# Kernel tuning notes

Hardware: AMD Instinct MI355X
Metric: run time of the kernel (lower is better)

The kernel has to match this reference:

```python
import jax, jax.numpy as jnp
import numpy as np

D = 256; NH = 8; NL = 4; NP = 4; NLAYERS = 6; DFF = 1024; DH = D // NH
B = 2
SHAPES = [(128, 128), (64, 64), (32, 32), (16, 16)]
S_TOTAL = sum(h * w for h, w in SHAPES)  # 21760


def setup_inputs() -> dict:
    key = jax.random.key(0)
    ks = iter(jax.random.split(key, 64))
    inp = {}
    for l, (h, w) in enumerate(SHAPES):
        inp[f"src{l}"] = jax.random.normal(next(ks), (B, D, h, w), jnp.float32)
        inp[f"pos{l}"] = jax.random.normal(next(ks), (B, D, h, w), jnp.float32)
    def p(shape):
        return jax.random.normal(next(ks), shape, jnp.float32) * 0.02
    inp["level_embed"] = p((NL, D))
    inp["Woff"] = p((NLAYERS, D, NH * NL * NP * 2)); inp["boff"] = p((NLAYERS, NH * NL * NP * 2))
    inp["Wattn"] = p((NLAYERS, D, NH * NL * NP)); inp["battn"] = p((NLAYERS, NH * NL * NP))
    inp["Wval"] = p((NLAYERS, D, D)); inp["bval"] = p((NLAYERS, D))
    inp["Wout"] = p((NLAYERS, D, D)); inp["bout"] = p((NLAYERS, D))
    inp["ln1_s"] = jnp.ones((NLAYERS, D)); inp["ln1_b"] = jnp.zeros((NLAYERS, D))
    inp["W1"] = p((NLAYERS, D, DFF)); inp["b1"] = p((NLAYERS, DFF))
    inp["W2"] = p((NLAYERS, DFF, D)); inp["b2"] = p((NLAYERS, D))
    inp["ln2_s"] = jnp.ones((NLAYERS, D)); inp["ln2_b"] = jnp.zeros((NLAYERS, D))
    return inp


def _layer_norm(x, s, b, eps=1e-5):
    m = jnp.mean(x, -1, keepdims=True)
    v = jnp.mean((x - m) ** 2, -1, keepdims=True)
    return (x - m) * jax.lax.rsqrt(v + eps) * s + b


def _ref_points(batch):
    # masks are all-False -> valid_ratios == 1, so reference points are just
    # normalized pixel centers, identical across the level axis.
    refs = []
    for h, w in SHAPES:
        yy, xx = jnp.meshgrid((jnp.arange(h) + 0.5) / h, (jnp.arange(w) + 0.5) / w, indexing="ij")
        refs.append(jnp.stack([xx.ravel(), yy.ravel()], -1))
    ref = jnp.concatenate(refs, 0)  # [S, 2] (x, y)
    return jnp.broadcast_to(ref[None, :, None, :], (batch, S_TOTAL, NL, 2))


def _ms_deform_attn(query, ref, src, Woff, boff, Wattn, battn, Wval, bval, Wout, bout):
    Bq, S, _ = query.shape
    value = (src @ Wval + bval).reshape(Bq, S, NH, DH)
    off = (query @ Woff + boff).reshape(Bq, S, NH, NL, NP, 2)
    aw = jax.nn.softmax((query @ Wattn + battn).reshape(Bq, S, NH, NL * NP), -1)
    aw = aw.reshape(Bq, S, NH, NL, NP)
    norm = jnp.array([[w, h] for h, w in SHAPES], dtype=query.dtype)  # [NL,2] = (W,H)
    loc = ref[:, :, None, :, None, :] + off / norm[None, None, None, :, None, :]  # [B,S,NH,NL,NP,2]
    out = jnp.zeros((Bq, NH, S, DH), query.dtype)
    start = 0
    for l, (h, w) in enumerate(SHAPES):
        v = value[:, start:start + h * w].transpose(0, 2, 1, 3)  # [B,NH,h*w,DH]
        start += h * w
        # grid_sample align_corners=False convention
        x = loc[:, :, :, l, :, 0] * w - 0.5  # [B,S,NH,NP]
        y = loc[:, :, :, l, :, 1] * h - 0.5
        x0 = jnp.floor(x); y0 = jnp.floor(y)
        lx = x - x0; ly = y - y0
        x0i = x0.astype(jnp.int32); y0i = y0.astype(jnp.int32)
        def tr(a):  # [B,S,NH,NP] -> [B,NH,S*NP,1]
            return a.transpose(0, 2, 1, 3).reshape(Bq, NH, S * NP, 1)
        def gather(xi, yi):
            ok = (xi >= 0) & (xi < w) & (yi >= 0) & (yi < h)
            idx = jnp.clip(yi, 0, h - 1) * w + jnp.clip(xi, 0, w - 1)
            idx = idx.transpose(0, 2, 1, 3).reshape(Bq, NH, S * NP)
            g = jnp.take_along_axis(v, idx[..., None], axis=2)  # [B,NH,S*NP,DH]
            return g * tr(ok).astype(v.dtype)  # zero padding outside
        samp = (tr((1 - lx) * (1 - ly)) * gather(x0i, y0i)
                + tr(lx * (1 - ly)) * gather(x0i + 1, y0i)
                + tr((1 - lx) * ly) * gather(x0i, y0i + 1)
                + tr(lx * ly) * gather(x0i + 1, y0i + 1))
        samp = (samp * tr(aw[:, :, :, l])).reshape(Bq, NH, S, NP, DH).sum(3)
        out = out + samp
    out = out.transpose(0, 2, 1, 3).reshape(Bq, S, D)
    return out @ Wout + bout


def _forward(srcs, poss, level_embed, Woff, boff, Wattn, battn, Wval, bval, Wout, bout,
             ln1_s, ln1_b, W1, b1, W2, b2, ln2_s, ln2_b):
    bsz = srcs[0].shape[0]
    src_flat = jnp.concatenate([s.reshape(bsz, D, -1).transpose(0, 2, 1) for s in srcs], 1)
    pos_flat = jnp.concatenate(
        [p.reshape(bsz, D, -1).transpose(0, 2, 1) + level_embed[l] for l, p in enumerate(poss)], 1)
    ref = _ref_points(bsz)
    out = src_flat
    for i in range(NLAYERS):
        q = out + pos_flat
        attn = _ms_deform_attn(q, ref, out, Woff[i], boff[i], Wattn[i], battn[i],
                               Wval[i], bval[i], Wout[i], bout[i])
        out = _layer_norm(out + attn, ln1_s[i], ln1_b[i])
        ff = jax.nn.relu(out @ W1[i] + b1[i]) @ W2[i] + b2[i]
        out = _layer_norm(out + ff, ln2_s[i], ln2_b[i])
    return out  # memory: [B, S_TOTAL, D]


def reference(src0, src1, src2, src3, pos0, pos1, pos2, pos3, level_embed,
              Woff, boff, Wattn, battn, Wval, bval, Wout, bout,
              ln1_s, ln1_b, W1, b1, W2, b2, ln2_s, ln2_b):
    return _forward([src0, src1, src2, src3], [pos0, pos1, pos2, pos3], level_embed,
                    Woff, boff, Wattn, battn, Wval, bval, Wout, bout,
                    ln1_s, ln1_b, W1, b1, W2, b2, ln2_s, ln2_b)
```

## Files before the change

kernel.cpp:

```cpp
#include <hip/hip_runtime.h>
#include <math.h>

#define DMODEL 256
#define NHEADS 8
#define NLAY 6
#define DFF 1024
#define DHEAD 32
#define NB 2
#define STOT 21760
#define MTOT (NB * STOT)

typedef unsigned short u16;
typedef __attribute__((ext_vector_type(8))) short short8;
typedef __attribute__((ext_vector_type(4))) float floatx4;

__device__ __forceinline__ float bf2f(u16 h) {
    unsigned int u = ((unsigned int)h) << 16;
    return __uint_as_float(u);
}
__device__ __forceinline__ u16 f2bf(float f) {
    unsigned int u = __float_as_uint(f);
    u = u + 0x7fffu + ((u >> 16) & 1u);
    return (u16)(u >> 16);
}

__global__ __launch_bounds__(256)
void biascat_kernel(const float* __restrict__ boff, const float* __restrict__ battn,
                    float* __restrict__ bias384)
{
    const int t = blockIdx.x * 256 + threadIdx.x;
    if (t >= NLAY * 384) return;
    const int i = t / 384, c = t - i * 384;
    bias384[t] = (c < 256) ? boff[i * 256 + c] : battn[i * 128 + (c - 256)];
}

__global__ __launch_bounds__(256)
void wtrans_kernel(const float* __restrict__ W, u16* __restrict__ Wt,
                   const int K, const int N, const long wstride, const long ostride)
{
    __shared__ float ts[32][33];
    W  += blockIdx.z * wstride;
    Wt += blockIdx.z * ostride;
    const int n0 = blockIdx.x * 32;
    const int k0 = blockIdx.y * 32;
    const int t = threadIdx.x;
    const int nl = t & 31, kl = t >> 5;
#pragma unroll
    for (int p = 0; p < 4; ++p) {
        const int k = kl + p * 8;
        ts[k][nl] = W[(long)(k0 + k) * N + n0 + nl];
    }
    __syncthreads();
    const int c = t & 31, r0 = t >> 5;
#pragma unroll
    for (int p = 0; p < 4; ++p) {
        const int r = r0 + p * 8;
        Wt[(long)(n0 + r) * K + k0 + c] = f2bf(ts[c][r]);
    }
}

__global__ __launch_bounds__(256)
void flatten_kernel(const float* __restrict__ src, const float* __restrict__ pos,
                    const float* __restrict__ le_row,
                    float* __restrict__ out, u16* __restrict__ outb,
                    u16* __restrict__ posb, u16* __restrict__ qb,
                    int HW, int start)
{
    __shared__ float ts[32][33];
    __shared__ float tp[32][33];
    const int b   = blockIdx.z;
    const int d0  = blockIdx.y * 32;
    const int hw0 = blockIdx.x * 32;
    const int t   = threadIdx.x;
    const int hwl = t & 31;
    const int dl  = t >> 5;
#pragma unroll
    for (int p = 0; p < 4; ++p) {
        const int dd = dl + p * 8;
        const int d  = d0 + dd;
        const long idx = ((long)(b * DMODEL + d)) * HW + hw0 + hwl;
        ts[dd][hwl] = src[idx];
        tp[dd][hwl] = pos[idx] + le_row[d];
    }
    __syncthreads();
    const int dl2  = t & 31;
    const int hwl2 = t >> 5;
#pragma unroll
    for (int p = 0; p < 4; ++p) {
        const int hh  = hwl2 + p * 8;
        const int tok = start + hw0 + hh;
        const long o  = ((long)(b * STOT + tok)) * DMODEL + d0 + dl2;
        const float v = ts[dl2][hh];
        const float pp = tp[dl2][hh];
        out[o]  = v;
        outb[o] = f2bf(v);
        posb[o] = f2bf(pp);
        qb[o]   = f2bf(v + pp);
    }
}

__global__ __launch_bounds__(256)
void mfma_gemm(const u16* __restrict__ A, const u16* __restrict__ Bt,
               const int ldb, const float* __restrict__ bias,
               u16* __restrict__ Cb, const int ldc, u16* __restrict__ Cb2,
               const int K, const int relu)
{
    __shared__ u16 As[128 * 40];
    __shared__ u16 Bs[128 * 40];
    const int tid  = threadIdx.x;
    const int wv   = tid >> 6;
    const int lane = tid & 63;
    const int m0 = blockIdx.y * 128;
    const int n0 = blockIdx.x * 128;
    const int wm = (wv & 1) * 64;
    const int wn = (wv >> 1) * 64;
    const int q   = lane >> 4;
    const int c16 = lane & 15;

    const int srow = tid >> 2;
    const int scol = (tid & 3) * 8;

    floatx4 acc[4][4];
#pragma unroll
    for (int i = 0; i < 4; ++i)
#pragma unroll
        for (int j = 0; j < 4; ++j)
            acc[i][j] = (floatx4){0.f, 0.f, 0.f, 0.f};

    union Frag { short8 v; uint2 u[2]; };

    for (int k0 = 0; k0 < K; k0 += 32) {
#pragma unroll
        for (int it = 0; it < 2; ++it) {
            const int r = srow + it * 64;
            const uint4 va = *(const uint4*)(A + (long)(m0 + r) * K + k0 + scol);
            uint2 lo, hi;
            lo.x = va.x; lo.y = va.y; hi.x = va.z; hi.y = va.w;
            *(uint2*)&As[r * 40 + scol]     = lo;
            *(uint2*)&As[r * 40 + scol + 4] = hi;
            const uint4 vb = *(const uint4*)(Bt + (long)(n0 + r) * ldb + k0 + scol);
            lo.x = vb.x; lo.y = vb.y; hi.x = vb.z; hi.y = vb.w;
            *(uint2*)&Bs[r * 40 + scol]     = lo;
            *(uint2*)&Bs[r * 40 + scol + 4] = hi;
        }
        __syncthreads();

        short8 af[4], bf[4];
#pragma unroll
        for (int i = 0; i < 4; ++i) {
            Frag fa;
            const int ao = (wm + i * 16 + c16) * 40 + q * 8;
            fa.u[0] = *(const uint2*)&As[ao];
            fa.u[1] = *(const uint2*)&As[ao + 4];
            af[i] = fa.v;
            Frag fb;
            const int bo = (wn + i * 16 + c16) * 40 + q * 8;
            fb.u[0] = *(const uint2*)&Bs[bo];
            fb.u[1] = *(const uint2*)&Bs[bo + 4];
            bf[i] = fb.v;
        }
#pragma unroll
        for (int i = 0; i < 4; ++i)
#pragma unroll
            for (int j = 0; j < 4; ++j)
                acc[i][j] = __builtin_amdgcn_mfma_f32_16x16x32_bf16(
                    af[i], bf[j], acc[i][j], 0, 0, 0);
        __syncthreads();
    }

    u16* cb  = Cb;
    int ldcb = ldc, csub = 0;
    if (Cb2 && n0 >= 256) { cb = Cb2; ldcb = 128; csub = 256; }

#pragma unroll
    for (int i = 0; i < 4; ++i) {
#pragma unroll
        for (int j = 0; j < 4; ++j) {
            const int col = n0 + wn + j * 16 + c16;
            const float bv = bias ? bias[col] : 0.f;
#pragma unroll
            for (int r = 0; r < 4; ++r) {
                const int row = m0 + wm + i * 16 + q * 4 + r;
                float v = acc[i][j][r] + bv;
                if (relu) v = fmaxf(v, 0.f);
                cb[(long)row * ldcb + col - csub] = f2bf(v);
            }
        }
    }
}

__global__ __launch_bounds__(256)
void sample_kernel(const u16* __restrict__ value, const u16* __restrict__ offb,
                   const u16* __restrict__ logit, u16* __restrict__ sb)
{
    constexpr int LW[4] = {128, 64, 32, 16};
    constexpr int SH[4] = {7, 6, 5, 4};
    constexpr int LS[4] = {0, 16384, 20480, 21504};

    const int t = threadIdx.x;
    const int tl = t >> 6;
    const int tid64 = t & 63;
    const int h = tid64 >> 3;
    const int lane8 = tid64 & 7;
    const int blk = blockIdx.x * 4 + tl;
    const int b = blk / STOT;
    const int s = blk - b * STOT;

    float refx, refy;
    if (s < 16384) {
        const int yy = s >> 7, xx = s & 127;
        refx = (xx + 0.5f) * (1.f / 128.f); refy = (yy + 0.5f) * (1.f / 128.f);
    } else if (s < 20480) {
        const int sl = s - 16384; const int yy = sl >> 6, xx = sl & 63;
        refx = (xx + 0.5f) * (1.f / 64.f);  refy = (yy + 0.5f) * (1.f / 64.f);
    } else if (s < 21504) {
        const int sl = s - 20480; const int yy = sl >> 5, xx = sl & 31;
        refx = (xx + 0.5f) * (1.f / 32.f);  refy = (yy + 0.5f) * (1.f / 32.f);
    } else {
        const int sl = s - 21504; const int yy = sl >> 4, xx = sl & 15;
        refx = (xx + 0.5f) * (1.f / 16.f);  refy = (yy + 0.5f) * (1.f / 16.f);
    }

    const uint* awp = (const uint*)(logit + (long)blk * 128 + h * 16);
    const uint4 la = ((const uint4*)awp)[0];
    const uint4 lb = ((const uint4*)awp)[1];
    const uint lu[8] = {la.x, la.y, la.z, la.w, lb.x, lb.y, lb.z, lb.w};
    float lv[16];
#pragma unroll
    for (int j = 0; j < 8; ++j) {
        lv[2 * j]     = bf2f((u16)(lu[j] & 0xffffu));
        lv[2 * j + 1] = bf2f((u16)(lu[j] >> 16));
    }
    float mx = lv[0];
#pragma unroll
    for (int i = 1; i < 16; ++i) mx = fmaxf(mx, lv[i]);
    float pw[16];
    float se = 0.f;
#pragma unroll
    for (int i = 0; i < 16; ++i) { pw[i] = __expf(lv[i] - mx); se += pw[i]; }
    const float inv = 1.f / se;

    const uint* offp = (const uint*)(offb + (long)blk * 256 + h * 32);
    const int ch = h * DHEAD + lane8 * 4;
    const u16* vtok = value + (long)b * STOT * DMODEL + ch;

    float a0 = 0.f, a1 = 0.f, a2 = 0.f, a3 = 0.f;
#pragma unroll
    for (int l = 0; l < 4; ++l) {
        const int lw = LW[l], sh = SH[l];
        const u16* vbase = vtok + (long)LS[l] * DMODEL;
        const uint4 olv = ((const uint4*)offp)[l];
        const uint ou[4] = {olv.x, olv.y, olv.z, olv.w};
        const float fx = refx * lw - 0.5f;
        const float fy = refy * lw - 0.5f;

        float w[16];
        int ofs[16];
#pragma unroll
        for (int p = 0; p < 4; ++p) {
            const uint o2 = ou[p];
            const float x = fx + bf2f((u16)(o2 & 0xffffu));
            const float y = fy + bf2f((u16)(o2 >> 16));
            const float x0f = floorf(x), y0f = floorf(y);
            const float lx = x - x0f, ly = y - y0f;
            const int x0 = (int)x0f, y0 = (int)y0f;
            const float aP = pw[l * 4 + p];
            const float wx0 = ((uint)x0 < (uint)lw) ? (1.f - lx) : 0.f;
            const float wx1 = ((uint)(x0 + 1) < (uint)lw) ? lx : 0.f;
            const float wy0 = ((uint)y0 < (uint)lw) ? (aP * (1.f - ly)) : 0.f;
            const float wy1 = ((uint)(y0 + 1) < (uint)lw) ? (aP * ly) : 0.f;
            const int xc0 = x0 & (lw - 1), xc1 = (x0 + 1) & (lw - 1);
            const int r0 = (y0 & (lw - 1)) << sh;
            const int r1 = ((y0 + 1) & (lw - 1)) << sh;
            w[p * 4 + 0] = wy0 * wx0; ofs[p * 4 + 0] = r0 + xc0;
            w[p * 4 + 1] = wy0 * wx1; ofs[p * 4 + 1] = r0 + xc1;
            w[p * 4 + 2] = wy1 * wx0; ofs[p * 4 + 2] = r1 + xc0;
            w[p * 4 + 3] = wy1 * wx1; ofs[p * 4 + 3] = r1 + xc1;
        }
        uint2 dv[16];
#pragma unroll
        for (int i = 0; i < 16; ++i)
            dv[i] = *(const uint2*)(vbase + ((long)ofs[i] << 8));
#pragma unroll
        for (int i = 0; i < 16; ++i) {
            const float wi = w[i];
            a0 = fmaf(wi, __uint_as_float(dv[i].x << 16), a0);
            a1 = fmaf(wi, __uint_as_float(dv[i].x & 0xffff0000u), a1);
            a2 = fmaf(wi, __uint_as_float(dv[i].y << 16), a2);
            a3 = fmaf(wi, __uint_as_float(dv[i].y & 0xffff0000u), a3);
        }
    }
    a0 *= inv; a1 *= inv; a2 *= inv; a3 *= inv;
    ushort4 r;
    r.x = f2bf(a0); r.y = f2bf(a1); r.z = f2bf(a2); r.w = f2bf(a3);
    *(ushort4*)(sb + (long)blk * DMODEL + ch) = r;
}

__global__ __launch_bounds__(256)
void ln_kernel(float* __restrict__ out, u16* __restrict__ outb,
               u16* __restrict__ qb, const u16* __restrict__ posb,
               const u16* __restrict__ db,
               const float* __restrict__ gamma, const float* __restrict__ beta)
{
    const int wave = threadIdx.x >> 6;
    const int lane = threadIdx.x & 63;
    const long tok = (long)blockIdx.x * 4 + wave;
    float* op = out + tok * DMODEL + lane * 4;
    const float4 xo = *(const float4*)op;
    const ushort4 d4 = *(const ushort4*)(db + tok * DMODEL + lane * 4);
    float x[4] = {xo.x + bf2f(d4.x), xo.y + bf2f(d4.y),
                  xo.z + bf2f(d4.z), xo.w + bf2f(d4.w)};

    float sum = x[0] + x[1] + x[2] + x[3];
#pragma unroll
    for (int o = 32; o >= 1; o >>= 1) sum += __shfl_xor(sum, o);
    const float mean = sum * (1.f / 256.f);

    float vs = 0.f;
#pragma unroll
    for (int i = 0; i < 4; ++i) { const float d2 = x[i] - mean; vs += d2 * d2; }
#pragma unroll
    for (int o = 32; o >= 1; o >>= 1) vs += __shfl_xor(vs, o);
    const float rstd = rsqrtf(vs * (1.f / 256.f) + 1e-5f);

    const float4 g  = *(const float4*)(gamma + lane * 4);
    const float4 be = *(const float4*)(beta + lane * 4);
    float r[4];
    r[0] = (x[0] - mean) * rstd * g.x + be.x;
    r[1] = (x[1] - mean) * rstd * g.y + be.y;
    r[2] = (x[2] - mean) * rstd * g.z + be.z;
    r[3] = (x[3] - mean) * rstd * g.w + be.w;
    float4 rf; rf.x = r[0]; rf.y = r[1]; rf.z = r[2]; rf.w = r[3];
    *(float4*)op = rf;
    ushort4 rb;
    rb.x = f2bf(r[0]); rb.y = f2bf(r[1]); rb.z = f2bf(r[2]); rb.w = f2bf(r[3]);
    *(ushort4*)(outb + tok * DMODEL + lane * 4) = rb;
    if (qb) {
        const ushort4 p4 = *(const ushort4*)(posb + tok * DMODEL + lane * 4);
        ushort4 qv;
        qv.x = f2bf(r[0] + bf2f(p4.x));
        qv.y = f2bf(r[1] + bf2f(p4.y));
        qv.z = f2bf(r[2] + bf2f(p4.z));
        qv.w = f2bf(r[3] + bf2f(p4.w));
        *(ushort4*)(qb + tok * DMODEL + lane * 4) = qv;
    }
}

extern "C" void kernel_launch(void* const* d_in, const int* in_sizes, int n_in,
                              void* d_out, int out_size, void* d_ws, size_t ws_size,
                              hipStream_t stream)
{
    const float* src[4] = {(const float*)d_in[0], (const float*)d_in[2],
                           (const float*)d_in[4], (const float*)d_in[6]};
    const float* pos[4] = {(const float*)d_in[1], (const float*)d_in[3],
                           (const float*)d_in[5], (const float*)d_in[7]};
    const float* level_embed = (const float*)d_in[8];
    const float* Woff  = (const float*)d_in[9];
    const float* boff  = (const float*)d_in[10];
    const float* Wattn = (const float*)d_in[11];
    const float* battn = (const float*)d_in[12];
    const float* Wval  = (const float*)d_in[13];
    const float* bval  = (const float*)d_in[14];
    const float* Wout  = (const float*)d_in[15];
    const float* bout  = (const float*)d_in[16];
    const float* ln1s  = (const float*)d_in[17];
    const float* ln1b  = (const float*)d_in[18];
    const float* W1    = (const float*)d_in[19];
    const float* b1    = (const float*)d_in[20];
    const float* W2    = (const float*)d_in[21];
    const float* b2    = (const float*)d_in[22];
    const float* ln2s  = (const float*)d_in[23];
    const float* ln2b  = (const float*)d_in[24];

    float* out = (float*)d_out;
    const long MD = (long)MTOT * DMODEL;

    u16* outb = (u16*)d_ws;
    u16* posb = outb + MD;
    u16* qb   = posb + MD;
    u16* db   = qb + MD;
    u16* vb   = db + MD;
    u16* offb = vb + MD;
    u16* awb  = offb + MD;
    u16* sb   = awb + MD / 2;
    u16* hb   = vb;
    u16* wts  = vb + 4 * MD;
    u16* Wvalt = wts;
    u16* Wofat = Wvalt + 6L * 256 * 256;
    u16* Woutt = Wofat + 6L * 384 * 256;
    u16* W1t   = Woutt + 6L * 256 * 256;
    u16* W2t   = W1t   + 6L * 1024 * 256;
    float* bias384 = (float*)(W2t + 6L * 1024 * 256);

    biascat_kernel<<<9, 256, 0, stream>>>(boff, battn, bias384);
    wtrans_kernel<<<dim3(8, 8, 6),  256, 0, stream>>>(Wval,  Wvalt, 256, 256,
                                                      65536, 65536);
    wtrans_kernel<<<dim3(8, 8, 6),  256, 0, stream>>>(Woff,  Wofat, 256, 256,
                                                      65536, 98304);
    wtrans_kernel<<<dim3(4, 8, 6),  256, 0, stream>>>(Wattn, Wofat + 256 * 256,
                                                      256, 128, 32768, 98304);
    wtrans_kernel<<<dim3(8, 8, 6),  256, 0, stream>>>(Wout,  Woutt, 256, 256,
                                                      65536, 65536);
    wtrans_kernel<<<dim3(32, 8, 6), 256, 0, stream>>>(W1,    W1t, 256, 1024,
                                                      262144, 262144);
    wtrans_kernel<<<dim3(8, 32, 6), 256, 0, stream>>>(W2,    W2t, 1024, 256,
                                                      262144, 262144);

    {
        const int HW[4] = {16384, 4096, 1024, 256};
        const int ST[4] = {0, 16384, 20480, 21504};
        for (int l = 0; l < 4; ++l) {
            dim3 g(HW[l] / 32, DMODEL / 32, NB);
            flatten_kernel<<<g, 256, 0, stream>>>(src[l], pos[l],
                                                  level_embed + l * DMODEL,
                                                  out, outb, posb, qb, HW[l], ST[l]);
        }
    }

    const dim3 g2(2, MTOT / 128);
    const dim3 g3(3, MTOT / 128);
    const dim3 g8(8, MTOT / 128);

    for (int i = 0; i < NLAY; ++i) {
        const u16* Wv  = Wvalt + (long)i * 256 * 256;
        const u16* Wqa = Wofat + (long)i * 384 * 256;
        const u16* Wou = Woutt + (long)i * 256 * 256;
        const u16* W1i = W1t   + (long)i * 1024 * 256;
        const u16* W2i = W2t   + (long)i * 256 * 1024;
        const float* bv  = bval + (long)i * 256;
        const float* bqa = bias384 + (long)i * 384;
        const float* bou = bout + (long)i * 256;
        const float* b1i = b1   + (long)i * DFF;
        const float* b2i = b2   + (long)i * 256;

        mfma_gemm<<<g2, 256, 0, stream>>>(outb, Wv, 256, bv,
                                          vb, 256, nullptr, 256, 0);
        mfma_gemm<<<g3, 256, 0, stream>>>(qb, Wqa, 256, bqa,
                                          offb, 256, awb, 256, 0);
        sample_kernel<<<MTOT / 4, 256, 0, stream>>>(vb, offb, awb, sb);
        mfma_gemm<<<g2, 256, 0, stream>>>(sb, Wou, 256, bou,
                                          db, 256, nullptr, 256, 0);
        ln_kernel<<<MTOT / 4, 256, 0, stream>>>(out, outb, nullptr, nullptr, db,
                                                ln1s + (long)i * 256,
                                                ln1b + (long)i * 256);
        mfma_gemm<<<g8, 256, 0, stream>>>(outb, W1i, 256, b1i,
                                          hb, 1024, nullptr, 256, 1);
        mfma_gemm<<<g2, 256, 0, stream>>>(hb, W2i, 1024, b2i,
                                          db, 256, nullptr, 1024, 0);
        ln_kernel<<<MTOT / 4, 256, 0, stream>>>(out, outb, qb, posb, db,
                                                ln2s + (long)i * 256,
                                                ln2b + (long)i * 256);
    }
}
```

Measured before the change: 2.043 ms.

## Remap deformable sampling so each lane gathers full head rows per point

The sampling kernel is reorganised. Each lane now owns two sampling points and gathers all 32 channels of a head per corner with 64-byte vector loads, instead of owning 4 channels and looping over all 16 points with 8-byte loads. Accumulation uses packed fp32 FMAs. Softmax is done with cross-lane shuffles over the 8 lanes of a head, and partial sums are reduced through LDS. The aim is fewer, wider gather transactions and less redundant address and weight math, at the cost of a 33 KB LDS buffer per block. That buffer may lower occupancy, and float4 LDS accesses at a padded 33-float row stride are not 16-byte aligned.

```diff
diff --git a/kernel.cpp b/kernel.cpp
--- a/kernel.cpp
+++ b/kernel.cpp
@@ -13,6 +13,7 @@
 typedef unsigned short u16;
 typedef __attribute__((ext_vector_type(8))) short short8;
 typedef __attribute__((ext_vector_type(4))) float floatx4;
+typedef __attribute__((ext_vector_type(2))) float float2v;
 
 __device__ __forceinline__ float bf2f(u16 h) {
     unsigned int u = ((unsigned int)h) << 16;
@@ -22,6 +23,16 @@
     unsigned int u = __float_as_uint(f);
     u = u + 0x7fffu + ((u >> 16) & 1u);
     return (u16)(u >> 16);
+}
+
+__device__ __forceinline__ void pkfma(float2v& acc, float2v a, float2v b) {
+    asm("v_pk_fma_f32 %0, %1, %2, %0" : "+v"(acc) : "v"(a), "v"(b));
+}
+__device__ __forceinline__ float2v unpk(unsigned int u) {
+    float2v r;
+    r.x = __uint_as_float(u << 16);
+    r.y = __uint_as_float(u & 0xffff0000u);
+    return r;
 }
 
 __global__ __launch_bounds__(256)
@@ -189,20 +200,70 @@
     }
 }
 
+__device__ __forceinline__ void point_corners(
+    float refx, float refy, unsigned int o2, float aP,
+    int k, unsigned int base, float w[4], unsigned int o[4])
+{
+    const int lw = 128 >> k;
+    const float flw = (float)lw;
+    const float x = refx * flw - 0.5f + bf2f((u16)(o2 & 0xffffu));
+    const float y = refy * flw - 0.5f + bf2f((u16)(o2 >> 16));
+    const float x0f = floorf(x), y0f = floorf(y);
+    const float lx = x - x0f, ly = y - y0f;
+    const int x0 = (int)x0f, y0 = (int)y0f;
+    const float wx0 = ((unsigned int)x0 < (unsigned int)lw) ? (1.f - lx) : 0.f;
+    const float wx1 = ((unsigned int)(x0 + 1) < (unsigned int)lw) ? lx : 0.f;
+    const float wy0 = ((unsigned int)y0 < (unsigned int)lw) ? (aP * (1.f - ly)) : 0.f;
+    const float wy1 = ((unsigned int)(y0 + 1) < (unsigned int)lw) ? (aP * ly) : 0.f;
+    const unsigned int xc0 = (unsigned int)(x0 & (lw - 1)) << 9;
+    const unsigned int xc1 = (unsigned int)((x0 + 1) & (lw - 1)) << 9;
+    const unsigned int r0 = (unsigned int)(y0 & (lw - 1)) << (16 - k);
+    const unsigned int r1 = (unsigned int)((y0 + 1) & (lw - 1)) << (16 - k);
+    w[0] = wy0 * wx0; o[0] = base + r0 + xc0;
+    w[1] = wy0 * wx1; o[1] = base + r0 + xc1;
+    w[2] = wy1 * wx0; o[2] = base + r1 + xc0;
+    w[3] = wy1 * wx1; o[3] = base + r1 + xc1;
+}
+
+__device__ __forceinline__ void corner_acc(const char* __restrict__ vp,
+                                           unsigned int o, float w,
+                                           float2v acc[16])
+{
+    const uint4 d0 = *(const uint4*)(vp + o);
+    const uint4 d1 = *(const uint4*)(vp + o + 16);
+    const uint4 d2 = *(const uint4*)(vp + o + 32);
+    const uint4 d3 = *(const uint4*)(vp + o + 48);
+    float2v w2; w2.x = w; w2.y = w;
+    pkfma(acc[0],  w2, unpk(d0.x));
+    pkfma(acc[1],  w2, unpk(d0.y));
+    pkfma(acc[2],  w2, unpk(d0.z));
+    pkfma(acc[3],  w2, unpk(d0.w));
+    pkfma(acc[4],  w2, unpk(d1.x));
+    pkfma(acc[5],  w2, unpk(d1.y));
+    pkfma(acc[6],  w2, unpk(d1.z));
+    pkfma(acc[7],  w2, unpk(d1.w));
+    pkfma(acc[8],  w2, unpk(d2.x));
+    pkfma(acc[9],  w2, unpk(d2.y));
+    pkfma(acc[10], w2, unpk(d2.z));
+    pkfma(acc[11], w2, unpk(d2.w));
+    pkfma(acc[12], w2, unpk(d3.x));
+    pkfma(acc[13], w2, unpk(d3.y));
+    pkfma(acc[14], w2, unpk(d3.z));
+    pkfma(acc[15], w2, unpk(d3.w));
+}
+
 __global__ __launch_bounds__(256)
 void sample_kernel(const u16* __restrict__ value, const u16* __restrict__ offb,
                    const u16* __restrict__ logit, u16* __restrict__ sb)
 {
-    constexpr int LW[4] = {128, 64, 32, 16};
-    constexpr int SH[4] = {7, 6, 5, 4};
-    constexpr int LS[4] = {0, 16384, 20480, 21504};
-
-    const int t = threadIdx.x;
-    const int tl = t >> 6;
-    const int tid64 = t & 63;
-    const int h = tid64 >> 3;
-    const int lane8 = tid64 & 7;
-    const int blk = blockIdx.x * 4 + tl;
+    __shared__ float red[4][64][33];
+
+    const int t  = threadIdx.x;
+    const int wv = t >> 6;
+    const int l  = t & 63;
+    const int h  = l >> 3;
+    const int q  = l & 7;
+    const int blk = blockIdx.x * 4 + wv;
     const int b = blk / STOT;
     const int s = blk - b * STOT;
 
@@ -221,79 +282,71 @@
         refx = (xx + 0.5f) * (1.f / 16.f);  refy = (yy + 0.5f) * (1.f / 16.f);
     }
 
-    const uint* awp = (const uint*)(logit + (long)blk * 128 + h * 16);
-    const uint4 la = ((const uint4*)awp)[0];
-    const uint4 lb = ((const uint4*)awp)[1];
-    const uint lu[8] = {la.x, la.y, la.z, la.w, lb.x, lb.y, lb.z, lb.w};
-    float lv[16];
+    const unsigned int* offp = (const unsigned int*)(offb + (long)blk * 256 + h * 32);
+    const unsigned int o2_0 = offp[q];
+    const unsigned int o2_1 = offp[q + 8];
+    const u16* lp = logit + (long)blk * 128 + h * 16;
+    const float l0 = bf2f(lp[q]);
+    const float l1 = bf2f(lp[q + 8]);
+
+    float m = fmaxf(l0, l1);
+    m = fmaxf(m, __shfl_xor(m, 1));
+    m = fmaxf(m, __shfl_xor(m, 2));
+    m = fmaxf(m, __shfl_xor(m, 4));
+    const float e0 = __expf(l0 - m);
+    const float e1 = __expf(l1 - m);
+    float se = e0 + e1;
+    se += __shfl_xor(se, 1);
+    se += __shfl_xor(se, 2);
+    se += __shfl_xor(se, 4);
+    const float inv = 1.f / se;
+    const float aP0 = e0 * inv;
+    const float aP1 = e1 * inv;
+
+    const int k0 = q >> 2;
+    const int k1 = k0 + 2;
+    const unsigned int LS0 = k0 ? 16384u : 0u;
+    const unsigned int LS1 = k0 ? 21504u : 20480u;
+    const unsigned int tb = (unsigned int)(b * STOT);
+    const unsigned int hb64 = (unsigned int)(h * 64);
+    const unsigned int base0 = (tb + LS0) * 512u + hb64;
+    const unsigned int base1 = (tb + LS1) * 512u + hb64;
+
+    float w0[4], w1[4];
+    unsigned int oo0[4], oo1[4];
+    point_corners(refx, refy, o2_0, aP0, k0, base0, w0, oo0);
+    point_corners(refx, refy, o2_1, aP1, k1, base1, w1, oo1);
+
+    float2v acc[16];
+#pragma unroll
+    for (int n = 0; n < 16; ++n) { acc[n].x = 0.f; acc[n].y = 0.f; }
+
+    const char* vp = (const char*)value;
+#pragma unroll
+    for (int c = 0; c < 4; ++c) corner_acc(vp, oo0[c], w0[c], acc);
+#pragma unroll
+    for (int c = 0; c < 4; ++c) corner_acc(vp, oo1[c], w1[c], acc);
+
+    float* myrow = red[wv][l];
+#pragma unroll
+    for (int c = 0; c < 8; ++c) {
+        float4 v4;
+        v4.x = acc[2 * c].x;     v4.y = acc[2 * c].y;
+        v4.z = acc[2 * c + 1].x; v4.w = acc[2 * c + 1].y;
+        *(float4*)(myrow + c * 4) = v4;
+    }
+    __builtin_amdgcn_wave_barrier();
+    const float* hrow = red[wv][h * 8];
+    float4 sum; sum.x = 0.f; sum.y = 0.f; sum.z = 0.f; sum.w = 0.f;
 #pragma unroll
     for (int j = 0; j < 8; ++j) {
-        lv[2 * j]     = bf2f((u16)(lu[j] & 0xffffu));
-        lv[2 * j + 1] = bf2f((u16)(lu[j] >> 16));
-    }
-    float mx = lv[0];
-#pragma unroll
-    for (int i = 1; i < 16; ++i) mx = fmaxf(mx, lv[i]);
-    float pw[16];
-    float se = 0.f;
-#pragma unroll
-    for (int i = 0; i < 16; ++i) { pw[i] = __expf(lv[i] - mx); se += pw[i]; }
-    const float inv = 1.f / se;
-
-    const uint* offp = (const uint*)(offb + (long)blk * 256 + h * 32);
-    const int ch = h * DHEAD + lane8 * 4;
-    const u16* vtok = value + (long)b * STOT * DMODEL + ch;
-
-    float a0 = 0.f, a1 = 0.f, a2 = 0.f, a3 = 0.f;
-#pragma unroll
-    for (int l = 0; l < 4; ++l) {
-        const int lw = LW[l], sh = SH[l];
-        const u16* vbase = vtok + (long)LS[l] * DMODEL;
-        const uint4 olv = ((const uint4*)offp)[l];
-        const uint ou[4] = {olv.x, olv.y, olv.z, olv.w};
-        const float fx = refx * lw - 0.5f;
-        const float fy = refy * lw - 0.5f;
-
-        float w[16];
-        int ofs[16];
-#pragma unroll
-        for (int p = 0; p < 4; ++p) {
-            const uint o2 = ou[p];
-            const float x = fx + bf2f((u16)(o2 & 0xffffu));
-            const float y = fy + bf2f((u16)(o2 >> 16));
-            const float x0f = floorf(x), y0f = floorf(y);
-            const float lx = x - x0f, ly = y - y0f;
-            const int x0 = (int)x0f, y0 = (int)y0f;
-            const float aP = pw[l * 4 + p];
-            const float wx0 = ((uint)x0 < (uint)lw) ? (1.f - lx) : 0.f;
-            const float wx1 = ((uint)(x0 + 1) < (uint)lw) ? lx : 0.f;
-            const float wy0 = ((uint)y0 < (uint)lw) ? (aP * (1.f - ly)) : 0.f;
-            const float wy1 = ((uint)(y0 + 1) < (uint)lw) ? (aP * ly) : 0.f;
-            const int xc0 = x0 & (lw - 1), xc1 = (x0 + 1) & (lw - 1);
-            const int r0 = (y0 & (lw - 1)) << sh;
-            const int r1 = ((y0 + 1) & (lw - 1)) << sh;
-            w[p * 4 + 0] = wy0 * wx0; ofs[p * 4 + 0] = r0 + xc0;
-            w[p * 4 + 1] = wy0 * wx1; ofs[p * 4 + 1] = r0 + xc1;
-            w[p * 4 + 2] = wy1 * wx0; ofs[p * 4 + 2] = r1 + xc0;
-            w[p * 4 + 3] = wy1 * wx1; ofs[p * 4 + 3] = r1 + xc1;
-        }
-        uint2 dv[16];
-#pragma unroll
-        for (int i = 0; i < 16; ++i)
-            dv[i] = *(const uint2*)(vbase + ((long)ofs[i] << 8));
-#pragma unroll
-        for (int i = 0; i < 16; ++i) {
-            const float wi = w[i];
-            a0 = fmaf(wi, __uint_as_float(dv[i].x << 16), a0);
-            a1 = fmaf(wi, __uint_as_float(dv[i].x & 0xffff0000u), a1);
-            a2 = fmaf(wi, __uint_as_float(dv[i].y << 16), a2);
-            a3 = fmaf(wi, __uint_as_float(dv[i].y & 0xffff0000u), a3);
-        }
-    }
-    a0 *= inv; a1 *= inv; a2 *= inv; a3 *= inv;
+        const float4 v = *(const float4*)(hrow + j * 33 + q * 4);
+        sum.x += v.x; sum.y += v.y; sum.z += v.z; sum.w += v.w;
+    }
+
     ushort4 r;
-    r.x = f2bf(a0); r.y = f2bf(a1); r.z = f2bf(a2); r.w = f2bf(a3);
-    *(ushort4*)(sb + (long)blk * DMODEL + ch) = r;
+    r.x = f2bf(sum.x); r.y = f2bf(sum.y); r.z = f2bf(sum.z); r.w = f2bf(sum.w);
+    *(ushort4*)(sb + (long)blk * DMODEL + h * 32 + q * 4) = r;
 }
 
 __global__ __launch_bounds__(256)
```

After: 2.139 ms. +4.7%, slower.
